# Performance work log

Hardware: AMD Instinct MI355X
Metric: run time of the kernel (lower is better)

## Reference

```python
import jax, jax.numpy as jnp
import numpy as np

B, N, C, H = 64, 300, 256, 8  # batch, patches (img 1x300, patch 1x1), dim, heads
STD = 0.02


def setup_inputs() -> dict:
    key = jax.random.key(0)
    ks = jax.random.split(key, 6)
    return {
        "x": jax.random.normal(ks[0], (B, N, C), jnp.float32),
        "Wqk": jax.random.normal(ks[1], (2 * C, C), jnp.float32) * STD,
        "Wv": jax.random.normal(ks[2], (C, C), jnp.float32) * STD,
        "Wpos": jax.random.normal(ks[3], (H, 3), jnp.float32) * STD,
        "bpos": jnp.zeros((H,), jnp.float32),
        "Wproj": jax.random.normal(ks[4], (C, C), jnp.float32) * STD,
        "bproj": jnp.zeros((C,), jnp.float32),
        "gating": jnp.ones((H,), jnp.float32),
    }


def _rel_indices(n):
    d = (jnp.arange(n)[None, :] - jnp.arange(n)[:, None]).astype(jnp.float32)
    return jnp.stack([d, jnp.zeros_like(d), d * d], axis=-1)  # [N, N, 3]


def reference(x, Wqk, Wv, Wpos, bpos, Wproj, bproj, gating):
    Bb, Nn, Cc = x.shape
    Hh = gating.shape[0]
    hd = Cc // Hh
    scale = hd ** -0.5

    qk = (x @ Wqk.T).reshape(Bb, Nn, 2, Hh, hd)
    q = qk[:, :, 0].transpose(0, 2, 1, 3)  # [B,H,N,hd]
    k = qk[:, :, 1].transpose(0, 2, 1, 3)

    patch_score = jax.nn.softmax(jnp.einsum('bhnd,bhmd->bhnm', q, k) * scale, axis=-1)

    rel = _rel_indices(Nn)                               # [N,N,3]
    pos_score = (rel @ Wpos.T + bpos).transpose(2, 0, 1)  # [H,N,N]
    pos_score = jax.nn.softmax(pos_score, axis=-1)

    g = jax.nn.sigmoid(gating)[None, :, None, None]       # [1,H,1,1]
    attn = (1.0 - g) * patch_score + g * pos_score[None]
    attn = attn / attn.sum(axis=-1, keepdims=True)

    v = (x @ Wv.T).reshape(Bb, Nn, Hh, hd).transpose(0, 2, 1, 3)  # [B,H,N,hd]
    out = jnp.einsum('bhnm,bhmd->bhnd', attn, v)
    out = out.transpose(0, 2, 1, 3).reshape(Bb, Nn, Cc)
    return out @ Wproj.T + bproj
```

## Files before the change

### kernel.cpp

```cpp
#include <hip/hip_runtime.h>


#define NSEQ 300
#define HEADS 8
#define HD 32

typedef short v8s __attribute__((ext_vector_type(8)));
typedef float v4f __attribute__((ext_vector_type(4)));
typedef unsigned int v4u __attribute__((ext_vector_type(4)));

__device__ __forceinline__ ushort f2bf(float f) {
    unsigned u = __float_as_uint(f);
    u = (u + 0x7FFFu + ((u >> 16) & 1u)) >> 16;
    return (ushort)u;
}

__device__ __forceinline__ unsigned pk2bf(float a, float b) {
    unsigned ua = __float_as_uint(a), ub = __float_as_uint(b);
    ua += 0x7FFFu + ((ua >> 16) & 1u);
    ub += 0x7FFFu + ((ub >> 16) & 1u);
    return __builtin_amdgcn_perm(ub, ua, 0x07060302);
}

__device__ __forceinline__ unsigned cvtpk(float a, float b) {
    unsigned r;
    asm("v_cvt_pk_bf16_f32 %0, %1, %2" : "=v"(r) : "v"(a), "v"(b));
    return r;
}

__device__ __forceinline__ float fexp2(float x) {
    float r; asm("v_exp_f32 %0, %1" : "=v"(r) : "v"(x)); return r;
}

__device__ __forceinline__ void gl_lds16(const ushort* g, ushort* l) {
    __builtin_amdgcn_global_load_lds(
        (const __attribute__((address_space(1))) void*)g,
        (__attribute__((address_space(3))) void*)l, 16, 0, 0);
}

__global__ __launch_bounds__(256) void prep_kernel(
    const float* __restrict__ x,
    const float* __restrict__ Wqk, const float* __restrict__ Wv,
    const float* __restrict__ Wproj, const float* __restrict__ Wpos,
    const float* __restrict__ bpos, const float* __restrict__ gating,
    ushort* __restrict__ x_bf, ushort* __restrict__ Wf,
    ushort* __restrict__ wproj_t, ushort* __restrict__ gpos)
{
    int bid = blockIdx.x, tid = threadIdx.x;
    if (bid < 2432) {
        int idx = bid * 256 + tid;
        int c8 = idx & 31;
        int mrow = idx >> 5;
        unsigned b = (unsigned)mrow / 304u;
        int r = mrow - (int)b * 304;
        v4u pk = {0u, 0u, 0u, 0u};
        if (r < 300) {
            const float* src = x + ((size_t)b * 300 + r) * 256 + c8 * 8;
            float4 f0 = *(const float4*)src;
            float4 f1 = *(const float4*)(src + 4);
            pk = (v4u){pk2bf(f0.x, f0.y), pk2bf(f0.z, f0.w),
                       pk2bf(f1.x, f1.y), pk2bf(f1.z, f1.w)};
        }
        *(v4u*)&x_bf[(size_t)mrow * 256 + c8 * 8] = pk;
        return;
    }
    if (bid < 3040) {
        int sub = bid - 2432;
        int h = sub / 76;
        int i = (sub % 76) * 4 + (tid >> 6);
        int lane = tid & 63;
        ushort* gr = gpos + ((size_t)h * 304 + i) * 320;
        if (i >= NSEQ) {
#pragma unroll
            for (int t = 0; t < 5; ++t) gr[lane + 64 * t] = 0;
            return;
        }
        float w0 = Wpos[h * 3 + 0], w2 = Wpos[h * 3 + 2], bb = bpos[h];
        float g = 1.f / (1.f + __expf(-gating[h]));
        float sv[5]; int jj[5]; float m2 = -1e30f;
#pragma unroll
        for (int t = 0; t < 5; ++t) {
            int pos = lane + 64 * t;
            int p = pos >> 5, rem = pos & 31;
            int qd = rem >> 3, r8 = rem & 7;
            int nt = 2 * p + (r8 >> 2);
            int j = nt * 16 + qd * 4 + (r8 & 3);
            jj[t] = j;
            float d = (float)(j - i);
            float lg = fmaf(w2, d * d, fmaf(w0, d, bb));
            sv[t] = (j < NSEQ) ? lg : -1e30f;
            m2 = fmaxf(m2, sv[t]);
        }
#pragma unroll
        for (int off = 32; off > 0; off >>= 1) m2 = fmaxf(m2, __shfl_xor(m2, off));
        float sum = 0.f;
#pragma unroll
        for (int t = 0; t < 5; ++t) { sv[t] = __expf(sv[t] - m2); sum += sv[t]; }
#pragma unroll
        for (int off = 32; off > 0; off >>= 1) sum += __shfl_xor(sum, off);
        float gi = g / sum;
#pragma unroll
        for (int t = 0; t < 5; ++t)
            gr[lane + 64 * t] = (jj[t] < NSEQ) ? f2bf(sv[t] * gi) : 0;
        return;
    }
    if (bid < 3136) {
        int idx = (bid - 3040) * 256 + tid;
        int c = idx & 7;
        int t = idx >> 3;
        int hk = t / 96;
        int wc = t - hk * 96;
        int h = hk >> 2, kt = hk & 3;
        const float* src;
        if (wc < 32)      src = Wqk + (size_t)(h * 32 + wc) * 256;
        else if (wc < 64) src = Wqk + (size_t)(256 + h * 32 + (wc - 32)) * 256;
        else              src = Wv + (size_t)(h * 32 + (wc - 64)) * 256;
        src += kt * 64 + c * 8;
        float4 f0 = *(const float4*)src;
        float4 f1 = *(const float4*)(src + 4);
        v4u pk = {pk2bf(f0.x, f0.y), pk2bf(f0.z, f0.w),
                  pk2bf(f1.x, f1.y), pk2bf(f1.z, f1.w)};
        *(v4u*)&Wf[((size_t)(hk * 96 + wc)) * 64 + ((c ^ (wc & 7)) * 8)] = pk;
        return;
    }
    {
        int idx = (bid - 3136) * 256 + tid;
        int m = idx >> 5, ck = idx & 31;
        const float* src = Wproj + (size_t)m * 256 + ck * 8;
        int rt = m >> 7, rr = m & 127, kt = ck >> 3, c = ck & 7;
        float4 f0 = *(const float4*)src;
        float4 f1 = *(const float4*)(src + 4);
        v4u pk = {pk2bf(f0.x, f0.y), pk2bf(f0.z, f0.w),
                  pk2bf(f1.x, f1.y), pk2bf(f1.z, f1.w)};
        *(v4u*)&wproj_t[((size_t)(rt * 4 + kt) * 128 + rr) * 64 + ((c ^ (rr & 7)) * 8)] = pk;
    }
}

__global__ __launch_bounds__(512, 4) void fused_qkv_attn(
    const ushort* __restrict__ x_bf, const ushort* __restrict__ Wf,
    const ushort* __restrict__ gpos, const float* __restrict__ gating,
    ushort* __restrict__ ot)
{
    __shared__ ushort smem[25600];
    ushort* Xs = smem;
    ushort* Wsh = smem + 19456;
    ushort* Ks = smem;
    ushort* Vt = smem + 12160;

    int bid = blockIdx.x, b = bid & 63, h = bid >> 6;
    int tid = threadIdx.x, wave = tid >> 6, lane = tid & 63, li = lane & 15, qd = lane >> 4;

    const ushort* xbb = x_bf + (size_t)b * 304 * 256;
    const ushort* wfh = Wf + (size_t)h * 4 * 6144;

    v4f acc[3][6];
#pragma unroll
    for (int i = 0; i < 3; ++i)
#pragma unroll
        for (int j = 0; j < 6; ++j) acc[i][j] = (v4f){0.f, 0.f, 0.f, 0.f};

    for (int kt = 0; kt < 4; ++kt) {
        gl_lds16(wfh + (size_t)kt * 6144 + tid * 8, Wsh + tid * 8);
        if (tid < 256)
            gl_lds16(wfh + (size_t)kt * 6144 + (512 + tid) * 8, Wsh + (512 + tid) * 8);
#pragma unroll
        for (int s = 0; s < 4; ++s) {
            int cch = s * 512 + tid;
            int r = cch >> 3, sl = cch & 7;
            gl_lds16(xbb + (size_t)r * 256 + kt * 64 + ((sl ^ (r & 7)) * 8),
                     Xs + cch * 8);
        }
        if (tid < 384) {
            int cch = 2048 + tid;
            int r = cch >> 3, sl = cch & 7;
            gl_lds16(xbb + (size_t)r * 256 + kt * 64 + ((sl ^ (r & 7)) * 8),
                     Xs + cch * 8);
        }
        __syncthreads();
#pragma unroll
        for (int kc = 0; kc < 64; kc += 32) {
            int cb = (kc >> 3) + qd;
            int cs = cb ^ (li & 7);
            v8s bw[6];
#pragma unroll
            for (int ct = 0; ct < 6; ++ct)
                bw[ct] = *(const v8s*)&Wsh[(ct * 16 + li) * 64 + cs * 8];
#pragma unroll
            for (int i = 0; i < 3; ++i) {
                int rt = wave + i * 8;
                if (rt < 19) {
                    v8s ax = *(const v8s*)&Xs[(rt * 16 + li) * 64 + cs * 8];
#pragma unroll
                    for (int ct = 0; ct < 6; ++ct)
                        acc[i][ct] = __builtin_amdgcn_mfma_f32_16x16x32_bf16(bw[ct], ax, acc[i][ct], 0, 0, 0);
                }
            }
        }
        __syncthreads();
    }

    const float QSC = 0.25503486063f;
    v4u q0 = {0,0,0,0}, q1 = {0,0,0,0}, q2 = {0,0,0,0};
    int srcA = ((qd & 1) << 5) + li;
    int srcB = srcA + 16;
    {
        int d = tid >> 4, s = tid & 15;
        Vt[d * 328 + 288 + (s >> 2) * 8 + 4 + (s & 3)] = 0;
    }
#pragma unroll
    for (int i = 0; i < 3; ++i) {
        int rt = wave + i * 8;
        if (rt < 19) {
            unsigned W00 = cvtpk(acc[i][0][0] * QSC, acc[i][0][1] * QSC);
            unsigned W01 = cvtpk(acc[i][0][2] * QSC, acc[i][0][3] * QSC);
            unsigned W10 = cvtpk(acc[i][1][0] * QSC, acc[i][1][1] * QSC);
            unsigned W11 = cvtpk(acc[i][1][2] * QSC, acc[i][1][3] * QSC);
            unsigned a0 = __shfl(W00, srcA), a1 = __shfl(W01, srcA);
            unsigned a2 = __shfl(W00, srcB), a3 = __shfl(W01, srcB);
            unsigned b0 = __shfl(W10, srcA), b1 = __shfl(W11, srcA);
            unsigned b2 = __shfl(W10, srcB), b3 = __shfl(W11, srcB);
            bool hi = (qd >= 2);
            v4u qq = {hi ? b0 : a0, hi ? b1 : a1, hi ? b2 : a2, hi ? b3 : a3};
            if (i == 0) q0 = qq; else if (i == 1) q1 = qq; else q2 = qq;

            int row = rt * 16 + li;
#pragma unroll
            for (int ct = 2; ct < 4; ++ct) {
                uint2 wk = {cvtpk(acc[i][ct][0], acc[i][ct][1]),
                            cvtpk(acc[i][ct][2], acc[i][ct][3])};
                *(uint2*)&Ks[row * 40 + (ct - 2) * 16 + qd * 4] = wk;
            }
            int vt_off = (rt >> 1) * 32 + ((li >> 2) * 8) + ((rt & 1) * 4) + (li & 3);
#pragma unroll
            for (int ct = 4; ct < 6; ++ct)
#pragma unroll
                for (int r = 0; r < 4; ++r)
                    Vt[((ct - 4) * 16 + qd * 4 + r) * 328 + vt_off] = f2bf(acc[i][ct][r]);
        }
    }
    float g = 1.f / (1.f + __expf(-gating[h]));
    float omg = 1.f - g;
    __syncthreads();

    const ushort* ksp0 = &Ks[li * 40 + qd * 8];
    const ushort* vtb0 = &Vt[li * 328 + qd * 8];
    const ushort* vtb1 = &Vt[(16 + li) * 328 + qd * 8];
    const v4f z4 = {0.f, 0.f, 0.f, 0.f};

#pragma unroll 1
    for (int rg = wave; rg < 19; rg += 8) {
        int i0 = rg * 16;
        v8s bq = __builtin_bit_cast(v8s, q0);
        const ushort* gp = gpos + ((size_t)h * 304 + (i0 + li)) * 320 + qd * 8;

        v4f Oe0 = z4, Oe1 = z4, Og0 = z4, Og1 = z4;
        float esum = 0.f;

        v8s ak0 = *(const v8s*)(ksp0);
        v8s ak1 = *(const v8s*)(ksp0 + 640);
        v8s vb0c = *(const v8s*)(vtb0);
        v8s vb1c = *(const v8s*)(vtb1);
        v8s agc = *(const v8s*)(gp);
        v8s agn = *(const v8s*)(gp + 32);
        v4f s0n = __builtin_amdgcn_mfma_f32_16x16x32_bf16(ak0, bq, z4, 0, 0, 0);
        v4f s1n = __builtin_amdgcn_mfma_f32_16x16x32_bf16(ak1, bq, z4, 0, 0, 0);

#pragma unroll 1
        for (int p = 0; p < 9; ++p) {
            v4f s0 = s0n, s1 = s1n;
            v8s b0 = vb0c, b1 = vb1c, ag = agc;
            agc = agn;
            int gt = (p < 7) ? p + 2 : 9;
            ak0 = *(const v8s*)(ksp0 + (2 * p + 2) * 640);
            ak1 = *(const v8s*)(ksp0 + (2 * p + 3) * 640);
            vb0c = *(const v8s*)(vtb0 + (p + 1) * 32);
            vb1c = *(const v8s*)(vtb1 + (p + 1) * 32);
            agn = *(const v8s*)(gp + gt * 32);
            s0n = __builtin_amdgcn_mfma_f32_16x16x32_bf16(ak0, bq, z4, 0, 0, 0);
            s1n = __builtin_amdgcn_mfma_f32_16x16x32_bf16(ak1, bq, z4, 0, 0, 0);

            float e0 = fexp2(s0[0]);
            float e1 = fexp2(s0[1]);
            float e2 = fexp2(s0[2]);
            float e3 = fexp2(s0[3]);
            float f0 = fexp2(s1[0]);
            float f1 = fexp2(s1[1]);
            float f2 = fexp2(s1[2]);
            float f3 = fexp2(s1[3]);
            esum += ((e0 + e1) + (e2 + e3)) + ((f0 + f1) + (f2 + f3));
            v8s ae = __builtin_bit_cast(v8s, (v4u){cvtpk(e0, e1), cvtpk(e2, e3),
                                                   cvtpk(f0, f1), cvtpk(f2, f3)});
            __builtin_amdgcn_s_setprio(1);
            Oe0 = __builtin_amdgcn_mfma_f32_16x16x32_bf16(ae, b0, Oe0, 0, 0, 0);
            Oe1 = __builtin_amdgcn_mfma_f32_16x16x32_bf16(ae, b1, Oe1, 0, 0, 0);
            Og0 = __builtin_amdgcn_mfma_f32_16x16x32_bf16(ag, b0, Og0, 0, 0, 0);
            Og1 = __builtin_amdgcn_mfma_f32_16x16x32_bf16(ag, b1, Og1, 0, 0, 0);
            __builtin_amdgcn_s_setprio(0);
        }
        {
            float e0 = fexp2(s0n[0]);
            float e1 = fexp2(s0n[1]);
            float e2 = fexp2(s0n[2]);
            float e3 = fexp2(s0n[3]);
            if (qd == 3) { e0 = e1 = e2 = e3 = 0.f; }
            esum += (e0 + e1) + (e2 + e3);
            v8s ae = __builtin_bit_cast(v8s, (v4u){cvtpk(e0, e1), cvtpk(e2, e3), 0u, 0u});
            Oe0 = __builtin_amdgcn_mfma_f32_16x16x32_bf16(ae, vb0c, Oe0, 0, 0, 0);
            Oe1 = __builtin_amdgcn_mfma_f32_16x16x32_bf16(ae, vb1c, Oe1, 0, 0, 0);
            Og0 = __builtin_amdgcn_mfma_f32_16x16x32_bf16(agc, vb0c, Og0, 0, 0, 0);
            Og1 = __builtin_amdgcn_mfma_f32_16x16x32_bf16(agc, vb1c, Og1, 0, 0, 0);
        }
        esum += __shfl_xor(esum, 16);
        esum += __shfl_xor(esum, 32);
        float ps = omg / esum;
        float psr[4];
#pragma unroll
        for (int r = 0; r < 4; ++r) psr[r] = __shfl(ps, qd * 4 + r);
#pragma unroll
        for (int r = 0; r < 4; ++r) {
            int row = i0 + qd * 4 + r;
            if (row < NSEQ) {
                int m = b * NSEQ + row;
                int rt = m >> 7, rr = m & 127;
                int c0 = (h & 1) * 4 + (li >> 3);
                int p2 = li & 7;
                size_t tb = ((size_t)(rt * 4 + (h >> 1)) * 128 + rr) * 64;
                ot[tb + ((c0 ^ (rr & 7)) * 8) + p2] = f2bf(fmaf(psr[r], Oe0[r], Og0[r]));
                ot[tb + (((c0 + 2) ^ (rr & 7)) * 8) + p2] = f2bf(fmaf(psr[r], Oe1[r], Og1[r]));
            }
        }
        q0 = q1; q1 = q2;
    }
}

__global__ __launch_bounds__(256, 4) void gemm_proj_mfma(
    const ushort* __restrict__ A, const ushort* __restrict__ Bw,
    const float* __restrict__ bias, float* __restrict__ out)
{
    __shared__ ushort As[64 * 64];
    __shared__ ushort Bs[128 * 64];
    int tid = threadIdx.x;
    int wave = tid >> 6, lane = tid & 63, li = lane & 15, qd = lane >> 4;
    int rh = wave >> 1, ch = wave & 1;
    int by = blockIdx.y;
    const ushort* gA = A + ((size_t)(by >> 1) * 4 * 128 + (by & 1) * 64) * 64;
    const ushort* gB = Bw + (size_t)blockIdx.x * 4 * 8192;

    v4f acc[2][4];
#pragma unroll
    for (int i = 0; i < 2; ++i)
#pragma unroll
        for (int j = 0; j < 4; ++j) acc[i][j] = (v4f){0.f, 0.f, 0.f, 0.f};

    for (int kt = 0; kt < 4; ++kt) {
#pragma unroll
        for (int s = 0; s < 2; ++s) {
            int cch = s * 256 + tid;
            gl_lds16(gA + (size_t)kt * 128 * 64 + cch * 8, As + cch * 8);
        }
#pragma unroll
        for (int s = 0; s < 4; ++s) {
            int cch = s * 256 + tid;
            gl_lds16(gB + (size_t)kt * 8192 + cch * 8, Bs + cch * 8);
        }
        __syncthreads();
#pragma unroll
        for (int kc = 0; kc < 64; kc += 32) {
            int cb = (kc >> 3) + qd;
            int cs = cb ^ (li & 7);
            v8s a[2], b[4];
#pragma unroll
            for (int mt = 0; mt < 2; ++mt)
                a[mt] = *(const v8s*)&As[(rh * 32 + mt * 16 + li) * 64 + cs * 8];
#pragma unroll
            for (int nt = 0; nt < 4; ++nt)
                b[nt] = *(const v8s*)&Bs[(ch * 64 + nt * 16 + li) * 64 + cs * 8];
#pragma unroll
            for (int mt = 0; mt < 2; ++mt)
#pragma unroll
                for (int nt = 0; nt < 4; ++nt)
                    acc[mt][nt] = __builtin_amdgcn_mfma_f32_16x16x32_bf16(b[nt], a[mt], acc[mt][nt], 0, 0, 0);
        }
        __syncthreads();
    }

#pragma unroll
    for (int mt = 0; mt < 2; ++mt) {
        int row = by * 64 + rh * 32 + mt * 16 + li;
#pragma unroll
        for (int nt = 0; nt < 4; ++nt) {
            int col = blockIdx.x * 128 + ch * 64 + nt * 16 + qd * 4;
            float4 bv = *(const float4*)&bias[col];
            float4 st = {acc[mt][nt][0] + bv.x, acc[mt][nt][1] + bv.y,
                         acc[mt][nt][2] + bv.z, acc[mt][nt][3] + bv.w};
            *(float4*)&out[(size_t)row * 256 + col] = st;
        }
    }
}

extern "C" void kernel_launch(void* const* d_in, const int* in_sizes, int n_in,
                              void* d_out, int out_size, void* d_ws, size_t ws_size,
                              hipStream_t stream) {
    const float* x      = (const float*)d_in[0];
    const float* Wqk    = (const float*)d_in[1];
    const float* Wv     = (const float*)d_in[2];
    const float* Wpos   = (const float*)d_in[3];
    const float* bpos   = (const float*)d_in[4];
    const float* Wproj  = (const float*)d_in[5];
    const float* bproj  = (const float*)d_in[6];
    const float* gating = (const float*)d_in[7];
    float* out = (float*)d_out;

    ushort* gpos     = (ushort*)d_ws;
    ushort* Wf       = gpos + 778240;
    ushort* wproj_t  = Wf + 196608;
    ushort* o_t      = wproj_t + 65536;
    ushort* x_bf     = o_t + 4915200;

    prep_kernel<<<3168, 256, 0, stream>>>(x, Wqk, Wv, Wproj, Wpos, bpos, gating,
                                          x_bf, Wf, wproj_t, gpos);
    fused_qkv_attn<<<512, 512, 0, stream>>>(x_bf, Wf, gpos, gating, o_t);
    gemm_proj_mfma<<<dim3(2, 300), 256, 0, stream>>>(o_t, wproj_t, bproj, out);
}
```

Baseline: 121.7 us.

## Double-buffer LDS loads in QKV and projection GEMMs to overlap copy with MFMA

The fused QKV/attention kernel now splits its K loop into eight 32-wide steps instead of four 64-wide ones. The prep kernel repacks the weights to match this layout. Each step uses two LDS buffers, so the next step's global-to-LDS loads are issued before computing on the current one. The projection GEMM gets the same double buffering over four steps and drops the trailing barrier. This hides load latency behind MFMA work, at the cost of more LDS in the projection GEMM (its launch bound drops to 3 blocks) and a narrower 4-chunk swizzle in the QKV stage.

After: 121.1 us. About the same (-0.4%).

```diff
diff --git a/kernel.cpp b/kernel.cpp
--- a/kernel.cpp
+++ b/kernel.cpp
@@ -106,21 +106,22 @@
     }
     if (bid < 3136) {
         int idx = (bid - 3040) * 256 + tid;
-        int c = idx & 7;
-        int t = idx >> 3;
-        int hk = t / 96;
-        int wc = t - hk * 96;
-        int h = hk >> 2, kt = hk & 3;
+        int s = idx & 3;
+        int t = idx >> 2;
+        int hst = t / 96;
+        int wc = t - hst * 96;
+        int st = hst & 7, h = hst >> 3;
+        int lc = s ^ (wc & 3);
         const float* src;
         if (wc < 32)      src = Wqk + (size_t)(h * 32 + wc) * 256;
         else if (wc < 64) src = Wqk + (size_t)(256 + h * 32 + (wc - 32)) * 256;
         else              src = Wv + (size_t)(h * 32 + (wc - 64)) * 256;
-        src += kt * 64 + c * 8;
+        src += st * 32 + lc * 8;
         float4 f0 = *(const float4*)src;
         float4 f1 = *(const float4*)(src + 4);
         v4u pk = {pk2bf(f0.x, f0.y), pk2bf(f0.z, f0.w),
                   pk2bf(f1.x, f1.y), pk2bf(f1.z, f1.w)};
-        *(v4u*)&Wf[((size_t)(hk * 96 + wc)) * 64 + ((c ^ (wc & 7)) * 8)] = pk;
+        *(v4u*)&Wf[((size_t)(hst * 96 + wc)) * 32 + s * 8] = pk;
         return;
     }
     {
@@ -142,8 +143,6 @@
     ushort* __restrict__ ot)
 {
     __shared__ ushort smem[25600];
-    ushort* Xs = smem;
-    ushort* Wsh = smem + 19456;
     ushort* Ks = smem;
     ushort* Vt = smem + 12160;
 
@@ -151,7 +150,7 @@
     int tid = threadIdx.x, wave = tid >> 6, lane = tid & 63, li = lane & 15, qd = lane >> 4;
 
     const ushort* xbb = x_bf + (size_t)b * 304 * 256;
-    const ushort* wfh = Wf + (size_t)h * 4 * 6144;
+    const ushort* wfh = Wf + (size_t)h * 24576;
 
     v4f acc[3][6];
 #pragma unroll
@@ -159,37 +158,46 @@
 #pragma unroll
         for (int j = 0; j < 6; ++j) acc[i][j] = (v4f){0.f, 0.f, 0.f, 0.f};
 
-    for (int kt = 0; kt < 4; ++kt) {
-        gl_lds16(wfh + (size_t)kt * 6144 + tid * 8, Wsh + tid * 8);
-        if (tid < 256)
-            gl_lds16(wfh + (size_t)kt * 6144 + (512 + tid) * 8, Wsh + (512 + tid) * 8);
-#pragma unroll
-        for (int s = 0; s < 4; ++s) {
-            int cch = s * 512 + tid;
-            int r = cch >> 3, sl = cch & 7;
-            gl_lds16(xbb + (size_t)r * 256 + kt * 64 + ((sl ^ (r & 7)) * 8),
-                     Xs + cch * 8);
-        }
-        if (tid < 384) {
-            int cch = 2048 + tid;
-            int r = cch >> 3, sl = cch & 7;
-            gl_lds16(xbb + (size_t)r * 256 + kt * 64 + ((sl ^ (r & 7)) * 8),
-                     Xs + cch * 8);
-        }
-        __syncthreads();
-#pragma unroll
-        for (int kc = 0; kc < 64; kc += 32) {
-            int cb = (kc >> 3) + qd;
-            int cs = cb ^ (li & 7);
+    {
+        ushort* Xb0 = smem;            ushort* Xb1 = smem + 9728;
+        ushort* Wb0 = smem + 19456;    ushort* Wb1 = smem + 22528;
+
+        auto issue_step = [&](int st, ushort* xb, ushort* wb) {
+#pragma unroll
+            for (int s = 0; s < 2; ++s) {
+                int cch = s * 512 + tid;
+                int r = cch >> 2, sl = cch & 3;
+                gl_lds16(xbb + (size_t)r * 256 + st * 32 + ((sl ^ (r & 3)) * 8),
+                         xb + cch * 8);
+            }
+            if (tid < 192) {
+                int cch = 1024 + tid;
+                int r = cch >> 2, sl = cch & 3;
+                gl_lds16(xbb + (size_t)r * 256 + st * 32 + ((sl ^ (r & 3)) * 8),
+                         xb + cch * 8);
+            }
+            if (tid < 384)
+                gl_lds16(wfh + st * 3072 + tid * 8, wb + tid * 8);
+        };
+
+        issue_step(0, Xb0, Wb0);
+#pragma unroll
+        for (int st = 0; st < 8; ++st) {
+            __syncthreads();
+            if (st < 7)
+                issue_step(st + 1, (st & 1) ? Xb0 : Xb1, (st & 1) ? Wb0 : Wb1);
+            const ushort* xb = (st & 1) ? Xb1 : Xb0;
+            const ushort* wb = (st & 1) ? Wb1 : Wb0;
+            int cs = qd ^ (li & 3);
             v8s bw[6];
 #pragma unroll
             for (int ct = 0; ct < 6; ++ct)
-                bw[ct] = *(const v8s*)&Wsh[(ct * 16 + li) * 64 + cs * 8];
+                bw[ct] = *(const v8s*)&wb[(ct * 16 + li) * 32 + cs * 8];
 #pragma unroll
             for (int i = 0; i < 3; ++i) {
                 int rt = wave + i * 8;
                 if (rt < 19) {
-                    v8s ax = *(const v8s*)&Xs[(rt * 16 + li) * 64 + cs * 8];
+                    v8s ax = *(const v8s*)&xb[(rt * 16 + li) * 32 + cs * 8];
 #pragma unroll
                     for (int ct = 0; ct < 6; ++ct)
                         acc[i][ct] = __builtin_amdgcn_mfma_f32_16x16x32_bf16(bw[ct], ax, acc[i][ct], 0, 0, 0);
@@ -333,12 +341,15 @@
     }
 }
 
-__global__ __launch_bounds__(256, 4) void gemm_proj_mfma(
+__global__ __launch_bounds__(256, 3) void gemm_proj_mfma(
     const ushort* __restrict__ A, const ushort* __restrict__ Bw,
     const float* __restrict__ bias, float* __restrict__ out)
 {
-    __shared__ ushort As[64 * 64];
-    __shared__ ushort Bs[128 * 64];
+    __shared__ ushort smem[24576];
+    ushort* As0 = smem;
+    ushort* As1 = smem + 4096;
+    ushort* Bs0 = smem + 8192;
+    ushort* Bs1 = smem + 16384;
     int tid = threadIdx.x;
     int wave = tid >> 6, lane = tid & 63, li = lane & 15, qd = lane >> 4;
     int rh = wave >> 1, ch = wave & 1;
@@ -352,18 +363,27 @@
 #pragma unroll
         for (int j = 0; j < 4; ++j) acc[i][j] = (v4f){0.f, 0.f, 0.f, 0.f};
 
-    for (int kt = 0; kt < 4; ++kt) {
+    auto issue_step = [&](int kt, ushort* as, ushort* bs) {
 #pragma unroll
         for (int s = 0; s < 2; ++s) {
             int cch = s * 256 + tid;
-            gl_lds16(gA + (size_t)kt * 128 * 64 + cch * 8, As + cch * 8);
+            gl_lds16(gA + (size_t)kt * 8192 + cch * 8, as + cch * 8);
         }
 #pragma unroll
         for (int s = 0; s < 4; ++s) {
             int cch = s * 256 + tid;
-            gl_lds16(gB + (size_t)kt * 8192 + cch * 8, Bs + cch * 8);
-        }
+            gl_lds16(gB + (size_t)kt * 8192 + cch * 8, bs + cch * 8);
+        }
+    };
+
+    issue_step(0, As0, Bs0);
+#pragma unroll
+    for (int kt = 0; kt < 4; ++kt) {
         __syncthreads();
+        if (kt < 3)
+            issue_step(kt + 1, (kt & 1) ? As0 : As1, (kt & 1) ? Bs0 : Bs1);
+        const ushort* as = (kt & 1) ? As1 : As0;
+        const ushort* bs = (kt & 1) ? Bs1 : Bs0;
 #pragma unroll
         for (int kc = 0; kc < 64; kc += 32) {
             int cb = (kc >> 3) + qd;
@@ -371,17 +391,16 @@
             v8s a[2], b[4];
 #pragma unroll
             for (int mt = 0; mt < 2; ++mt)
-                a[mt] = *(const v8s*)&As[(rh * 32 + mt * 16 + li) * 64 + cs * 8];
+                a[mt] = *(const v8s*)&as[(rh * 32 + mt * 16 + li) * 64 + cs * 8];
 #pragma unroll
             for (int nt = 0; nt < 4; ++nt)
-                b[nt] = *(const v8s*)&Bs[(ch * 64 + nt * 16 + li) * 64 + cs * 8];
+                b[nt] = *(const v8s*)&bs[(ch * 64 + nt * 16 + li) * 64 + cs * 8];
 #pragma unroll
             for (int mt = 0; mt < 2; ++mt)
 #pragma unroll
                 for (int nt = 0; nt < 4; ++nt)
                     acc[mt][nt] = __builtin_amdgcn_mfma_f32_16x16x32_bf16(b[nt], a[mt], acc[mt][nt], 0, 0, 0);
         }
-        __syncthreads();
     }
 
 #pragma unroll
```
